# Performance work log

Measured on AMD Instinct MI355X. Metric: run time of the kernel, lower is better.

Reference implementation:

```python
import jax, jax.numpy as jnp
import numpy as np
from jax import lax

NUM_CLASSES = 21
KSIZE = 11
DIL = 1
BLUR = 4
NUM_STEPS = 5
YX_SCALE = 80.0
RGB_SCALE = 13.0
POS_SCALE = 3.0


def _ceil_pad_factor(sizes, factor):
    offs = tuple((factor - s % factor) % factor for s in sizes)
    return tuple((o + 1) // 2 for o in offs)


def avg_pool_nopad(x, k, pad):
    # F.avg_pool2d(kernel=stride=k, padding=pad, count_include_pad=False)
    pcfg = ((0, 0), (0, 0), (pad[0], pad[0]), (pad[1], pad[1]))
    s = lax.reduce_window(x, jnp.float32(0), lax.add, (1, 1, k, k), (1, 1, k, k), pcfg)
    ones = jnp.ones((1, 1) + x.shape[2:], x.dtype)
    cnt = lax.reduce_window(ones, jnp.float32(0), lax.add, (1, 1, k, k), (1, 1, k, k), pcfg)
    return s / cnt


def _patches(x, k, dil):
    # im2col with zero padding (matches torch F.unfold used by pac)
    pad = (k // 2) * dil
    p = lax.conv_general_dilated_patches(
        x, (k, k), (1, 1), [(pad, pad), (pad, pad)], rhs_dilation=(dil, dil))
    B, C, H, W = x.shape
    return p.reshape(B, C, k * k, H, W)


def gaussian_kernel(feat, k, dil):
    # pixel-adaptive Gaussian kernel: exp(-0.5 * ||f_i - f_j||^2) over the KxK window
    p = _patches(feat, k, dil)                       # [B,F,k2,H,W]
    d = p - feat[:, :, None]
    return jnp.exp(-0.5 * jnp.sum(d * d, axis=1))    # [B,k2,H,W]


def pac_message(Q, kernel, k, dil):
    # shared-filter (Potts, spatial_filter=False) pac conv: per-channel kernel-weighted sum
    p = _patches(Q, k, dil)                          # [B,C,k2,h,w]
    return jnp.einsum('bckhw,bkhw->bchw', p, kernel)


def upsample_bilinear(x, scale):
    # matches F.interpolate(mode='bilinear', align_corners=False)
    B, C, h, w = x.shape
    def idx_w(n_in):
        n_out = n_in * scale
        src = jnp.clip((jnp.arange(n_out, dtype=jnp.float32) + 0.5) / scale - 0.5, 0.0, n_in - 1.0)
        i0 = jnp.floor(src).astype(jnp.int32)
        i1 = jnp.minimum(i0 + 1, n_in - 1)
        return i0, i1, (src - i0).astype(x.dtype)
    y0, y1, wy = idx_w(h)
    x0, x1, wx = idx_w(w)
    xh = x[:, :, y0, :] * (1 - wy)[None, None, :, None] + x[:, :, y1, :] * wy[None, None, :, None]
    return xh[:, :, :, x0] * (1 - wx)[None, None, None, :] + xh[:, :, :, x1] * wx[None, None, None, :]


def crf_forward(x, w_backbone, b_backbone, unary_weight, pairwise_weights):
    B, _, H, W = x.shape
    # backbone stub: 3x3 conv producing unary logits [B,21,H,W]
    unary = lax.conv_general_dilated(
        x, w_backbone, (1, 1), [(1, 1), (1, 1)],
        dimension_numbers=('NCHW', 'OIHW', 'NCHW')) + b_backbone[None, :, None, None]
    # edge features: bilateral (YX/80, RGB/13) and spatial (YX/3)
    yx = jnp.stack(jnp.meshgrid(jnp.arange(H, dtype=x.dtype), jnp.arange(W, dtype=x.dtype), indexing='ij'))
    yx = jnp.broadcast_to(yx[None], (B, 2, H, W))
    feat_bilateral = jnp.concatenate([yx / YX_SCALE, x / RGB_SCALE], axis=1)  # [B,5,H,W]
    feat_spatial = yx / POS_SCALE                                             # [B,2,H,W]
    pad = _ceil_pad_factor((H, W), BLUR)
    kernels = [gaussian_kernel(avg_pool_nopad(f, BLUR, pad), KSIZE, DIL)
               for f in (feat_bilateral, feat_spatial)]

    def step(logQ, unary, k1, k2, uw, pw):
        Q = jax.nn.softmax(logQ, axis=1)
        Qb = avg_pool_nopad(Q, BLUR, pad)
        new = uw * unary
        for kern, w in ((k1, pw[0]), (k2, pw[1])):
            msg = pac_message(Qb, kern, KSIZE, DIL)
            msg = upsample_bilinear(msg, BLUR)[:, :, pad[0]:pad[0] + H, pad[1]:pad[1] + W]
            new = new + w * msg
        return new

    logQ = unary
    for _ in range(NUM_STEPS):
        logQ = step(logQ, unary, kernels[0], kernels[1], unary_weight, pairwise_weights)
    return logQ  # final_output == 'log_Q'


def setup_inputs():
    key = jax.random.key(0)
    ks = jax.random.split(key, 3)
    B, H, W = 2, 512, 512
    x = jax.random.uniform(ks[0], (B, 3, H, W), jnp.float32) * 255.0  # image in [0,255]
    w_backbone = jax.random.normal(ks[1], (NUM_CLASSES, 3, 3, 3), jnp.float32) * 0.1
    b_backbone = jax.random.normal(ks[2], (NUM_CLASSES,), jnp.float32) * 0.01
    unary_weight = jnp.asarray(0.8, jnp.float32)
    pairwise_weights = jnp.asarray([2.0, 0.6], jnp.float32)
    return {"x": x, "w_backbone": w_backbone, "b_backbone": b_backbone,
            "unary_weight": unary_weight, "pairwise_weights": pairwise_weights}


def reference(x, w_backbone, b_backbone, unary_weight, pairwise_weights):
    return crf_forward(x, w_backbone, b_backbone, unary_weight, pairwise_weights)
```

## Files before the change

### kernel.cpp

```cpp
#include <hip/hip_runtime.h>

#define NCH 21
#define HWP (1 << 14)
#define KS 11
#define KK 121
#define PTW 32
#define PTH 8
#define LROW 48
#define LHGT 18
#define LPLANE (LROW * LHGT)

__global__ __launch_bounds__(256) void k_conv_sm(const float* __restrict__ x,
                                                 const float* __restrict__ w,
                                                 const float* __restrict__ bias,
                                                 float* __restrict__ unary,
                                                 float* __restrict__ qb) {
    int idx = blockIdx.x * 256 + threadIdx.x;
    int r = idx & 3;
    int xqi = (idx >> 2) & 127;
    int py = (idx >> 9) & 127;
    int b = idx >> 16;
    int y = 4 * py + r;
    int xq = xqi << 2;

    float p[3][3][6];
#pragma unroll
    for (int ch = 0; ch < 3; ++ch) {
        const float* xp = x + (((size_t)(b * 3 + ch)) << 18);
#pragma unroll
        for (int rr = 0; rr < 3; ++rr) {
            int yy = y + rr - 1;
            if ((unsigned)yy >= 512u) {
#pragma unroll
                for (int j = 0; j < 6; ++j) p[ch][rr][j] = 0.f;
            } else {
                const float* row = xp + (yy << 9);
                float4 v = *(const float4*)(row + xq);
                p[ch][rr][1] = v.x; p[ch][rr][2] = v.y; p[ch][rr][3] = v.z; p[ch][rr][4] = v.w;
                p[ch][rr][0] = (xq > 0) ? row[xq - 1] : 0.f;
                p[ch][rr][5] = (xq + 4 < 512) ? row[xq + 4] : 0.f;
            }
        }
    }
    float a[NCH][4];
    for (int o = 0; o < NCH; ++o) {
        const float* wp = w + o * 27;
        float bz = bias[o];
        float a0 = bz, a1 = bz, a2 = bz, a3 = bz;
#pragma unroll
        for (int ch = 0; ch < 3; ++ch)
#pragma unroll
            for (int rr = 0; rr < 3; ++rr) {
                float w0 = wp[ch * 9 + rr * 3 + 0];
                float w1 = wp[ch * 9 + rr * 3 + 1];
                float w2 = wp[ch * 9 + rr * 3 + 2];
                const float* pr = p[ch][rr];
                a0 += w0 * pr[0] + w1 * pr[1] + w2 * pr[2];
                a1 += w0 * pr[1] + w1 * pr[2] + w2 * pr[3];
                a2 += w0 * pr[2] + w1 * pr[3] + w2 * pr[4];
                a3 += w0 * pr[3] + w1 * pr[4] + w2 * pr[5];
            }
        *(float4*)(unary + (((size_t)(b * NCH + o)) << 18) + (y << 9) + xq) =
            make_float4(a0, a1, a2, a3);
        a[o][0] = a0; a[o][1] = a1; a[o][2] = a2; a[o][3] = a3;
    }
    float qsum[NCH];
#pragma unroll
    for (int c = 0; c < NCH; ++c) qsum[c] = 0.f;
#pragma unroll
    for (int i2 = 0; i2 < 4; ++i2) {
        float m = a[0][i2];
#pragma unroll
        for (int c = 1; c < NCH; ++c) m = fmaxf(m, a[c][i2]);
        float s = 0.f;
#pragma unroll
        for (int c = 0; c < NCH; ++c) { float e = __expf(a[c][i2] - m); a[c][i2] = e; s += e; }
        float inv = 1.0f / s;
#pragma unroll
        for (int c = 0; c < NCH; ++c) qsum[c] += a[c][i2] * inv;
    }
#pragma unroll
    for (int c = 0; c < NCH; ++c) {
        float v = qsum[c];
        v += __shfl_xor(v, 1);
        v += __shfl_xor(v, 2);
        if (r == 0) qb[(((size_t)(b * NCH + c)) << 14) + (py << 7) + xqi] = v * 0.0625f;
    }
}

__global__ __launch_bounds__(256) void k_pool_rgb(const float* __restrict__ x,
                                                  float* __restrict__ prgb) {
    int idx = blockIdx.x * 256 + threadIdx.x;
    int p = idx & (HWP - 1);
    int ch = (idx >> 14) % 3;
    int b = idx / (3 * HWP);
    int py = p >> 7, px = p & 127;
    const float* xp = x + (((size_t)(b * 3 + ch)) << 18);
    float s = 0.f;
#pragma unroll
    for (int r = 0; r < 4; ++r) {
        const float4 v = *(const float4*)(xp + (((4 * py + r) << 9) + 4 * px));
        s += v.x + v.y + v.z + v.w;
    }
    prgb[idx] = s * 0.0625f;
}

__global__ __launch_bounds__(256) void k_build_kc(const float* __restrict__ prgb,
                                                  const float* __restrict__ pw,
                                                  float* __restrict__ kc) {
    int idx = blockIdx.x * 256 + threadIdx.x;
    int p = idx & (HWP - 1);
    int jj = idx >> 14;
    int b = (jj >= KK) ? 1 : 0;
    int j = jj - KK * b;
    int dy = j / KS, dx = j - dy * KS;
    int py = p >> 7, px = p & 127;
    float pw0 = pw[0], pw1 = pw[1];

    const float inv13 = 1.0f / 13.0f;
    float fy = (4.f * py + 1.5f) * (1.0f / 80.0f);
    float fx = (4.f * px + 1.5f) * (1.0f / 80.0f);
    const float* pb = prgb + (size_t)b * 3 * HWP;
    float r0 = pb[p] * inv13;
    float g0 = pb[HWP + p] * inv13;
    float b0 = pb[2 * HWP + p] * inv13;
    float sy = (4.f * py + 1.5f) * (1.0f / 3.0f);
    float sx = (4.f * px + 1.5f) * (1.0f / 3.0f);

    int ny = py + dy - 5;
    int nx = px + dx - 5;
    float s1, s2;
    if ((unsigned)ny < 128u && (unsigned)nx < 128u) {
        int np = (ny << 7) + nx;
        float r2 = pb[np] * inv13;
        float g2 = pb[HWP + np] * inv13;
        float b2 = pb[2 * HWP + np] * inv13;
        float dya = fy - (4.f * ny + 1.5f) * (1.0f / 80.0f);
        float dxa = fx - (4.f * nx + 1.5f) * (1.0f / 80.0f);
        float dr = r0 - r2, dg = g0 - g2, db = b0 - b2;
        s1 = dya * dya + dxa * dxa + dr * dr + dg * dg + db * db;
        float dys = sy - (4.f * ny + 1.5f) * (1.0f / 3.0f);
        float dxs = sx - (4.f * nx + 1.5f) * (1.0f / 3.0f);
        s2 = dys * dys + dxs * dxs;
    } else {
        s1 = fy * fy + fx * fx + r0 * r0 + g0 * g0 + b0 * b0;
        s2 = sy * sy + sx * sx;
    }
    kc[idx] = pw0 * __expf(-0.5f * s1) + pw1 * __expf(-0.5f * s2);
}

__global__ __launch_bounds__(256) void k_pac4(const float* __restrict__ qb,
                                              const float* __restrict__ kc,
                                              float* __restrict__ msgc) {
    int tile = blockIdx.x & 63;
    int cg = (blockIdx.x >> 6) % 6;
    int b = blockIdx.x / 384;
    int tx0 = (tile & 3) * PTW;
    int ty0 = (tile >> 2) * PTH;
    int c0 = cg * 4;

    __shared__ float lq[4 * LPLANE];

    const float* qbb = qb + (((size_t)(b * NCH)) << 14);
    for (int i = threadIdx.x; i < 4 * LPLANE; i += 256) {
        int c = i / LPLANE;
        int rem = i - c * LPLANE;
        int ly = rem / LROW;
        int lx = rem - ly * LROW;
        int ch = c0 + c;
        int gy = ty0 + ly - 5, gx = tx0 + lx - 5;
        float v = 0.f;
        if (ch < NCH && lx < 42 && (unsigned)gy < 128u && (unsigned)gx < 128u)
            v = qbb[((size_t)ch << 14) + (gy << 7) + gx];
        lq[i] = v;
    }
    __syncthreads();

    int s = threadIdx.x & 63;
    int cl = threadIdx.x >> 6;
    int my = s >> 3;
    int mx0 = (s & 7) << 2;
    int ch = c0 + cl;

    float acc0 = 0.f, acc1 = 0.f, acc2 = 0.f, acc3 = 0.f;
    int p0 = ((ty0 + my) << 7) + tx0 + mx0;
    const float* kcb = kc + (((size_t)(b * KK)) << 14) + p0;
    const float* lbase = lq + cl * LPLANE + mx0;

    for (int dy = 0; dy < KS; ++dy) {
        const float* lp = lbase + (my + dy) * LROW;
        float4 v0 = *(const float4*)(lp + 0);
        float4 v1 = *(const float4*)(lp + 4);
        float4 v2 = *(const float4*)(lp + 8);
        float4 v3 = *(const float4*)(lp + 12);
        float rb[16] = {v0.x, v0.y, v0.z, v0.w, v1.x, v1.y, v1.z, v1.w,
                        v2.x, v2.y, v2.z, v2.w, v3.x, v3.y, v3.z, v3.w};
        const float* kcrow = kcb + (((size_t)(dy * KS)) << 14);
#pragma unroll
        for (int dx = 0; dx < KS; ++dx) {
            float4 k4 = *(const float4*)(kcrow + (((size_t)dx) << 14));
            acc0 += k4.x * rb[dx + 0];
            acc1 += k4.y * rb[dx + 1];
            acc2 += k4.z * rb[dx + 2];
            acc3 += k4.w * rb[dx + 3];
        }
    }
    if (ch < NCH)
        *(float4*)(msgc + (((size_t)(b * NCH + ch)) << 14) + p0) =
            make_float4(acc0, acc1, acc2, acc3);
}

__global__ __launch_bounds__(256) void k_step(const float* __restrict__ unary,
                                              const float* __restrict__ msgc,
                                              const float* __restrict__ uwp,
                                              float* __restrict__ qb,
                                              float* __restrict__ out,
                                              int write_out) {
    int idx = blockIdx.x * 256 + threadIdx.x;
    int r = idx & 3;
    int px = (idx >> 2) & 127;
    int py = (idx >> 9) & 127;
    int b = idx >> 16;
    int y = 4 * py + r;
    float uw = uwp[0];

    int rA = (r < 2) ? max(py - 1, 0) : py;
    int rB = (r < 2) ? py : min(py + 1, 127);
    float fy = (r == 0) ? 0.625f : (r == 1) ? 0.875f : (r == 2) ? 0.125f : 0.375f;
    int xm1 = max(px - 1, 0), xp1 = min(px + 1, 127);
    int oA = rA << 7, oB = rB << 7;

    size_t base = (((size_t)(b * NCH)) << 18) + (y << 9) + (px << 2);
    const float* up = unary + base;
    const float* mp = msgc + (((size_t)(b * NCH)) << 14);

    float a[NCH][4];
#pragma unroll
    for (int c = 0; c < NCH; ++c) {
        float4 u4 = *(const float4*)(up + ((size_t)c << 18));
        const float* m0 = mp + ((size_t)c << 14);
        float aL = m0[oA + xm1], aM = m0[oA + px], aR = m0[oA + xp1];
        float bL = m0[oB + xm1], bM = m0[oB + px], bR = m0[oB + xp1];
        float cL = aL + (bL - aL) * fy;
        float cM = aM + (bM - aM) * fy;
        float cR = aR + (bR - aR) * fy;
        a[c][0] = uw * u4.x + cL + (cM - cL) * 0.625f;
        a[c][1] = uw * u4.y + cL + (cM - cL) * 0.875f;
        a[c][2] = uw * u4.z + cM + (cR - cM) * 0.125f;
        a[c][3] = uw * u4.w + cM + (cR - cM) * 0.375f;
    }

    if (write_out) {
        float* op = out + base;
#pragma unroll
        for (int c = 0; c < NCH; ++c)
            *(float4*)(op + ((size_t)c << 18)) = make_float4(a[c][0], a[c][1], a[c][2], a[c][3]);
        return;
    }

    float qsum[NCH];
#pragma unroll
    for (int c = 0; c < NCH; ++c) qsum[c] = 0.f;
#pragma unroll
    for (int i2 = 0; i2 < 4; ++i2) {
        float m = a[0][i2];
#pragma unroll
        for (int c = 1; c < NCH; ++c) m = fmaxf(m, a[c][i2]);
        float ss = 0.f;
#pragma unroll
        for (int c = 0; c < NCH; ++c) { float e = __expf(a[c][i2] - m); a[c][i2] = e; ss += e; }
        float inv = 1.0f / ss;
#pragma unroll
        for (int c = 0; c < NCH; ++c) qsum[c] += a[c][i2] * inv;
    }
#pragma unroll
    for (int c = 0; c < NCH; ++c) {
        float v = qsum[c];
        v += __shfl_xor(v, 1);
        v += __shfl_xor(v, 2);
        if (r == 0) qb[(((size_t)(b * NCH + c)) << 14) + (py << 7) + px] = v * 0.0625f;
    }
}

extern "C" void kernel_launch(void* const* d_in, const int* in_sizes, int n_in,
                              void* d_out, int out_size, void* d_ws, size_t ws_size,
                              hipStream_t stream) {
    const float* x  = (const float*)d_in[0];
    const float* wb = (const float*)d_in[1];
    const float* bb = (const float*)d_in[2];
    const float* uw = (const float*)d_in[3];
    const float* pw = (const float*)d_in[4];
    float* out = (float*)d_out;

    float* ws    = (float*)d_ws;
    float* unary = ws;
    float* kc    = unary + 11010048;
    float* qb    = kc + 3964928;
    float* msgc  = qb + 688128;
    float* prgb  = msgc;

    k_conv_sm<<<512, 256, 0, stream>>>(x, wb, bb, unary, qb);
    k_pool_rgb<<<384, 256, 0, stream>>>(x, prgb);
    k_build_kc<<<15488, 256, 0, stream>>>(prgb, pw, kc);

    for (int s = 0; s < 5; ++s) {
        k_pac4<<<768, 256, 0, stream>>>(qb, kc, msgc);
        k_step<<<512, 256, 0, stream>>>(unary, msgc, uw, qb, out, (s == 4) ? 1 : 0);
    }
}
```

Measured before the change: 284.0 us.

## Recompute unary conv in step kernel, store kernel weights in fp16, widen pac blocks

The stored 21-channel unary tensor (about 44MB) is dropped. k_step now recomputes the 3x3 backbone conv from the image patch, which trades extra FLOPs for far less HBM traffic on every step. The PAC kernel-weight tensor is stored in fp16, halving its bandwidth at some loss of precision. The pac kernel now runs 512-thread blocks covering 8 channels each, so each loaded kc value is reused across twice as many channels.

New measurement: 340.4 us. 1.2x slower.

```diff
diff --git a/kernel.cpp b/kernel.cpp
--- a/kernel.cpp
+++ b/kernel.cpp
@@ -10,20 +10,10 @@
 #define LHGT 18
 #define LPLANE (LROW * LHGT)
 
-__global__ __launch_bounds__(256) void k_conv_sm(const float* __restrict__ x,
-                                                 const float* __restrict__ w,
-                                                 const float* __restrict__ bias,
-                                                 float* __restrict__ unary,
-                                                 float* __restrict__ qb) {
-    int idx = blockIdx.x * 256 + threadIdx.x;
-    int r = idx & 3;
-    int xqi = (idx >> 2) & 127;
-    int py = (idx >> 9) & 127;
-    int b = idx >> 16;
-    int y = 4 * py + r;
-    int xq = xqi << 2;
-
-    float p[3][3][6];
+typedef _Float16 half4 __attribute__((ext_vector_type(4)));
+
+__device__ __forceinline__ void load_patch(const float* __restrict__ x, int b, int y,
+                                           int xq, float p[3][3][6]) {
 #pragma unroll
     for (int ch = 0; ch < 3; ++ch) {
         const float* xp = x + (((size_t)(b * 3 + ch)) << 18);
@@ -42,28 +32,48 @@
             }
         }
     }
+}
+
+__device__ __forceinline__ void conv4(const float p[3][3][6], const float* __restrict__ w,
+                                      const float* __restrict__ bias, int o,
+                                      float& a0, float& a1, float& a2, float& a3) {
+    const float* wp = w + o * 27;
+    float bz = bias[o];
+    a0 = bz; a1 = bz; a2 = bz; a3 = bz;
+#pragma unroll
+    for (int ch = 0; ch < 3; ++ch)
+#pragma unroll
+        for (int rr = 0; rr < 3; ++rr) {
+            float w0 = wp[ch * 9 + rr * 3 + 0];
+            float w1 = wp[ch * 9 + rr * 3 + 1];
+            float w2 = wp[ch * 9 + rr * 3 + 2];
+            const float* pr = p[ch][rr];
+            a0 += w0 * pr[0] + w1 * pr[1] + w2 * pr[2];
+            a1 += w0 * pr[1] + w1 * pr[2] + w2 * pr[3];
+            a2 += w0 * pr[2] + w1 * pr[3] + w2 * pr[4];
+            a3 += w0 * pr[3] + w1 * pr[4] + w2 * pr[5];
+        }
+}
+
+__global__ __launch_bounds__(256) void k_init_q(const float* __restrict__ x,
+                                                const float* __restrict__ w,
+                                                const float* __restrict__ bias,
+                                                float* __restrict__ qb) {
+    int idx = blockIdx.x * 256 + threadIdx.x;
+    int r = idx & 3;
+    int px = (idx >> 2) & 127;
+    int py = (idx >> 9) & 127;
+    int b = idx >> 16;
+    int y = 4 * py + r;
+    int xq = px << 2;
+
+    float p[3][3][6];
+    load_patch(x, b, y, xq, p);
+
     float a[NCH][4];
-    for (int o = 0; o < NCH; ++o) {
-        const float* wp = w + o * 27;
-        float bz = bias[o];
-        float a0 = bz, a1 = bz, a2 = bz, a3 = bz;
-#pragma unroll
-        for (int ch = 0; ch < 3; ++ch)
-#pragma unroll
-            for (int rr = 0; rr < 3; ++rr) {
-                float w0 = wp[ch * 9 + rr * 3 + 0];
-                float w1 = wp[ch * 9 + rr * 3 + 1];
-                float w2 = wp[ch * 9 + rr * 3 + 2];
-                const float* pr = p[ch][rr];
-                a0 += w0 * pr[0] + w1 * pr[1] + w2 * pr[2];
-                a1 += w0 * pr[1] + w1 * pr[2] + w2 * pr[3];
-                a2 += w0 * pr[2] + w1 * pr[3] + w2 * pr[4];
-                a3 += w0 * pr[3] + w1 * pr[4] + w2 * pr[5];
-            }
-        *(float4*)(unary + (((size_t)(b * NCH + o)) << 18) + (y << 9) + xq) =
-            make_float4(a0, a1, a2, a3);
-        a[o][0] = a0; a[o][1] = a1; a[o][2] = a2; a[o][3] = a3;
-    }
+    for (int o = 0; o < NCH; ++o)
+        conv4(p, w, bias, o, a[o][0], a[o][1], a[o][2], a[o][3]);
+
     float qsum[NCH];
 #pragma unroll
     for (int c = 0; c < NCH; ++c) qsum[c] = 0.f;
@@ -84,7 +94,7 @@
         float v = qsum[c];
         v += __shfl_xor(v, 1);
         v += __shfl_xor(v, 2);
-        if (r == 0) qb[(((size_t)(b * NCH + c)) << 14) + (py << 7) + xqi] = v * 0.0625f;
+        if (r == 0) qb[(((size_t)(b * NCH + c)) << 14) + (py << 7) + px] = v * 0.0625f;
     }
 }
 
@@ -107,7 +117,7 @@
 
 __global__ __launch_bounds__(256) void k_build_kc(const float* __restrict__ prgb,
                                                   const float* __restrict__ pw,
-                                                  float* __restrict__ kc) {
+                                                  _Float16* __restrict__ kc) {
     int idx = blockIdx.x * 256 + threadIdx.x;
     int p = idx & (HWP - 1);
     int jj = idx >> 14;
@@ -146,23 +156,23 @@
         s1 = fy * fy + fx * fx + r0 * r0 + g0 * g0 + b0 * b0;
         s2 = sy * sy + sx * sx;
     }
-    kc[idx] = pw0 * __expf(-0.5f * s1) + pw1 * __expf(-0.5f * s2);
-}
-
-__global__ __launch_bounds__(256) void k_pac4(const float* __restrict__ qb,
-                                              const float* __restrict__ kc,
-                                              float* __restrict__ msgc) {
+    kc[idx] = (_Float16)(pw0 * __expf(-0.5f * s1) + pw1 * __expf(-0.5f * s2));
+}
+
+__global__ __launch_bounds__(512) void k_pac(const float* __restrict__ qb,
+                                             const _Float16* __restrict__ kc,
+                                             float* __restrict__ msgc) {
     int tile = blockIdx.x & 63;
-    int cg = (blockIdx.x >> 6) % 6;
-    int b = blockIdx.x / 384;
+    int cg = (blockIdx.x >> 6) % 3;
+    int b = blockIdx.x / 192;
     int tx0 = (tile & 3) * PTW;
     int ty0 = (tile >> 2) * PTH;
-    int c0 = cg * 4;
-
-    __shared__ float lq[4 * LPLANE];
+    int c0 = cg * 8;
+
+    __shared__ float lq[8 * LPLANE];
 
     const float* qbb = qb + (((size_t)(b * NCH)) << 14);
-    for (int i = threadIdx.x; i < 4 * LPLANE; i += 256) {
+    for (int i = threadIdx.x; i < 8 * LPLANE; i += 512) {
         int c = i / LPLANE;
         int rem = i - c * LPLANE;
         int ly = rem / LROW;
@@ -184,7 +194,7 @@
 
     float acc0 = 0.f, acc1 = 0.f, acc2 = 0.f, acc3 = 0.f;
     int p0 = ((ty0 + my) << 7) + tx0 + mx0;
-    const float* kcb = kc + (((size_t)(b * KK)) << 14) + p0;
+    const _Float16* kcb = kc + (((size_t)(b * KK)) << 14) + p0;
     const float* lbase = lq + cl * LPLANE + mx0;
 
     for (int dy = 0; dy < KS; ++dy) {
@@ -195,14 +205,14 @@
         float4 v3 = *(const float4*)(lp + 12);
         float rb[16] = {v0.x, v0.y, v0.z, v0.w, v1.x, v1.y, v1.z, v1.w,
                         v2.x, v2.y, v2.z, v2.w, v3.x, v3.y, v3.z, v3.w};
-        const float* kcrow = kcb + (((size_t)(dy * KS)) << 14);
+        const _Float16* kcrow = kcb + (((size_t)(dy * KS)) << 14);
 #pragma unroll
         for (int dx = 0; dx < KS; ++dx) {
-            float4 k4 = *(const float4*)(kcrow + (((size_t)dx) << 14));
-            acc0 += k4.x * rb[dx + 0];
-            acc1 += k4.y * rb[dx + 1];
-            acc2 += k4.z * rb[dx + 2];
-            acc3 += k4.w * rb[dx + 3];
+            half4 k4 = *(const half4*)(kcrow + (((size_t)dx) << 14));
+            acc0 += (float)k4.x * rb[dx + 0];
+            acc1 += (float)k4.y * rb[dx + 1];
+            acc2 += (float)k4.z * rb[dx + 2];
+            acc3 += (float)k4.w * rb[dx + 3];
         }
     }
     if (ch < NCH)
@@ -210,7 +220,9 @@
             make_float4(acc0, acc1, acc2, acc3);
 }
 
-__global__ __launch_bounds__(256) void k_step(const float* __restrict__ unary,
+__global__ __launch_bounds__(256) void k_step(const float* __restrict__ x,
+                                              const float* __restrict__ w,
+                                              const float* __restrict__ bias,
                                               const float* __restrict__ msgc,
                                               const float* __restrict__ uwp,
                                               float* __restrict__ qb,
@@ -222,7 +234,11 @@
     int py = (idx >> 9) & 127;
     int b = idx >> 16;
     int y = 4 * py + r;
+    int xq = px << 2;
     float uw = uwp[0];
+
+    float p[3][3][6];
+    load_patch(x, b, y, xq, p);
 
     int rA = (r < 2) ? max(py - 1, 0) : py;
     int rB = (r < 2) ? py : min(py + 1, 127);
@@ -230,28 +246,27 @@
     int xm1 = max(px - 1, 0), xp1 = min(px + 1, 127);
     int oA = rA << 7, oB = rB << 7;
 
-    size_t base = (((size_t)(b * NCH)) << 18) + (y << 9) + (px << 2);
-    const float* up = unary + base;
     const float* mp = msgc + (((size_t)(b * NCH)) << 14);
 
     float a[NCH][4];
 #pragma unroll
     for (int c = 0; c < NCH; ++c) {
-        float4 u4 = *(const float4*)(up + ((size_t)c << 18));
+        float u0, u1, u2, u3;
+        conv4(p, w, bias, c, u0, u1, u2, u3);
         const float* m0 = mp + ((size_t)c << 14);
         float aL = m0[oA + xm1], aM = m0[oA + px], aR = m0[oA + xp1];
         float bL = m0[oB + xm1], bM = m0[oB + px], bR = m0[oB + xp1];
         float cL = aL + (bL - aL) * fy;
         float cM = aM + (bM - aM) * fy;
         float cR = aR + (bR - aR) * fy;
-        a[c][0] = uw * u4.x + cL + (cM - cL) * 0.625f;
-        a[c][1] = uw * u4.y + cL + (cM - cL) * 0.875f;
-        a[c][2] = uw * u4.z + cM + (cR - cM) * 0.125f;
-        a[c][3] = uw * u4.w + cM + (cR - cM) * 0.375f;
+        a[c][0] = uw * u0 + cL + (cM - cL) * 0.625f;
+        a[c][1] = uw * u1 + cL + (cM - cL) * 0.875f;
+        a[c][2] = uw * u2 + cM + (cR - cM) * 0.125f;
+        a[c][3] = uw * u3 + cM + (cR - cM) * 0.375f;
     }
 
     if (write_out) {
-        float* op = out + base;
+        float* op = out + (((size_t)(b * NCH)) << 18) + (y << 9) + xq;
 #pragma unroll
         for (int c = 0; c < NCH; ++c)
             *(float4*)(op + ((size_t)c << 18)) = make_float4(a[c][0], a[c][1], a[c][2], a[c][3]);
@@ -292,19 +307,17 @@
     const float* pw = (const float*)d_in[4];
     float* out = (float*)d_out;
 
-    float* ws    = (float*)d_ws;
-    float* unary = ws;
-    float* kc    = unary + 11010048;
-    float* qb    = kc + 3964928;
+    _Float16* kc = (_Float16*)d_ws;
+    float* qb    = (float*)(kc + 3964928);
     float* msgc  = qb + 688128;
-    float* prgb  = msgc;
-
-    k_conv_sm<<<512, 256, 0, stream>>>(x, wb, bb, unary, qb);
+    float* prgb  = msgc + 688128;
+
+    k_init_q<<<512, 256, 0, stream>>>(x, wb, bb, qb);
     k_pool_rgb<<<384, 256, 0, stream>>>(x, prgb);
     k_build_kc<<<15488, 256, 0, stream>>>(prgb, pw, kc);
 
     for (int s = 0; s < 5; ++s) {
-        k_pac4<<<768, 256, 0, stream>>>(qb, kc, msgc);
-        k_step<<<512, 256, 0, stream>>>(unary, msgc, uw, qb, out, (s == 4) ? 1 : 0);
-    }
-}
+        k_pac<<<384, 512, 0, stream>>>(qb, kc, msgc);
+        k_step<<<512, 256, 0, stream>>>(x, wb, bb, msgc, uw, qb, out, (s == 4) ? 1 : 0);
+    }
+}
```
